# Performance work log

Hardware: AMD Instinct MI355X
Metric: run time of the kernel (lower is better)

The kernel has to match this reference:

```python
import jax, jax.numpy as jnp
import numpy as np

N, E, D, H, L, G, C = 50000, 800000, 128, 128, 3, 128, 10
BN_EPS = 1e-5


def setup_inputs() -> dict:
    key = jax.random.key(0)
    ks = jax.random.split(key, 16)
    inp = {
        "x": jax.random.normal(ks[0], (N, D), dtype=jnp.float32),
        "node_centrality": jax.random.uniform(ks[1], (N,), dtype=jnp.float32),
        "edge_centrality": jax.random.uniform(ks[2], (E,), dtype=jnp.float32),
        # stacked per-layer MLP params (in == hidden so stackable)
        "W1": jax.random.normal(ks[3], (L, D, H), dtype=jnp.float32) * 0.05,
        "b1": jnp.zeros((L, H), dtype=jnp.float32),
        "g1": jnp.ones((L, H), dtype=jnp.float32),
        "be1": jnp.zeros((L, H), dtype=jnp.float32),
        "W2": jax.random.normal(ks[4], (L, H, H), dtype=jnp.float32) * 0.05,
        "b2": jnp.zeros((L, H), dtype=jnp.float32),
        "Wc": jax.random.normal(ks[5], (H, C), dtype=jnp.float32) * 0.05,
        "bc": jnp.zeros((C,), dtype=jnp.float32),
        "edge_index": jax.random.randint(ks[6], (2, E), 0, N, dtype=jnp.int64),
        "batch": jnp.sort(jax.random.randint(ks[7], (N,), 0, G, dtype=jnp.int64)),
    }
    return inp


def _gin_forward(x, node_centrality, edge_centrality, W1, b1, g1, be1, W2, b2, Wc, bc, edge_index, batch):
    src, dst = edge_index[0], edge_index[1]  # x_j = x[src], aggregate at dst
    ec = edge_centrality[:, None]
    nc = node_centrality[:, None]
    for l in range(L):
        # message: gather + scale by edge centrality; aggr='add': scatter-add
        msg = x[src] * ec                                      # [E, H]
        agg = jax.ops.segment_sum(msg, dst, num_segments=N)    # [N, H]
        h = agg * nc + x                                       # (1 + eps) * x_r, eps = 0
        # MLP([in, hidden, hidden]): Linear -> BatchNorm(train) -> ReLU -> Linear
        h = h @ W1[l] + b1[l]
        mu = h.mean(axis=0)
        var = h.var(axis=0)  # biased, matches BN training stats
        h = (h - mu) * jax.lax.rsqrt(var + BN_EPS) * g1[l] + be1[l]
        h = jax.nn.relu(h)
        h = h @ W2[l] + b2[l]
        x = jax.nn.relu(h)  # outer .relu() in GIN.forward
    # global mean pool over graphs
    sums = jax.ops.segment_sum(x, batch, num_segments=G)           # [G, H]
    cnt = jax.ops.segment_sum(jnp.ones((N,), x.dtype), batch, num_segments=G)
    pooled = sums / jnp.maximum(cnt, 1.0)[:, None]
    return pooled @ Wc + bc  # [G, C]


def reference(x, edge_index, batch, node_centrality, edge_centrality, W1, b1, g1, be1, W2, b2, Wc, bc):
    return _gin_forward(x, node_centrality, edge_centrality, W1, b1, g1, be1, W2, b2, Wc, bc, edge_index, batch)
```

## Files before the change

### kernel.cpp

```cpp
#include <hip/hip_runtime.h>
#include <hip/hip_fp16.h>

#define Nn 50000
#define Ee 800000
#define HD 128
#define Ll 3
#define Gg 128
#define Cc 10
#define BN_EPS 1e-5f
#define NBLK1 782
#define NPART 1564
#define PPAD 1600
#define NSCB 49

typedef __attribute__((ext_vector_type(8))) __bf16 bf16x8;
typedef __attribute__((ext_vector_type(4))) __bf16 bf16x4;
typedef __attribute__((ext_vector_type(2))) __bf16 bf16x2;
typedef __attribute__((ext_vector_type(4))) float f32x4;

__global__ void k_deg(const int* __restrict__ dst, int* __restrict__ deg) {
  int i = blockIdx.x * blockDim.x + threadIdx.x;
  int base = i * 4;
  if (base >= Ee) return;
#pragma unroll
  for (int j = 0; j < 4; ++j) {
    int e = base + j;
    if (e < Ee) atomicAdd(&deg[dst[e]], 1);
  }
}

__global__ void k_scan1(const int* __restrict__ deg, int* __restrict__ offs,
                        int* __restrict__ bsum) {
  __shared__ int b0[1024], b1[1024];
  int tid = threadIdx.x;
  int i = blockIdx.x * 1024 + tid;
  int v = (i < Nn) ? deg[i] : 0;
  int* cur = b0; int* nxt = b1;
  cur[tid] = v;
  __syncthreads();
  for (int off = 1; off < 1024; off <<= 1) {
    int s = cur[tid] + ((tid >= off) ? cur[tid - off] : 0);
    nxt[tid] = s;
    __syncthreads();
    int* t = cur; cur = nxt; nxt = t;
  }
  if (i < Nn) offs[i] = cur[tid] - v;
  if (tid == 1023) bsum[blockIdx.x] = cur[1023];
}

__global__ void k_scan2(const int* __restrict__ bsum, int* __restrict__ carry) {
  int lane = threadIdx.x;
  int v = (lane < NSCB) ? bsum[lane] : 0;
  int s = v;
  for (int off = 1; off < 64; off <<= 1) {
    int t = __shfl_up(s, off, 64);
    if (lane >= off) s += t;
  }
  if (lane < NSCB) carry[lane] = s - v;
}

__global__ void k_scan3(const int* __restrict__ carry, int* __restrict__ offs,
                        int* __restrict__ cursor) {
  int i = blockIdx.x * 1024 + threadIdx.x;
  if (i < Nn) {
    int o = offs[i] + carry[blockIdx.x];
    offs[i] = o; cursor[i] = o;
  }
  if (i == 0) offs[Nn] = Ee;
}

__global__ void k_fill(const int* __restrict__ src, const int* __restrict__ dst,
                       const float* __restrict__ ec, int* __restrict__ cursor,
                       unsigned int* __restrict__ epk) {
  int i = blockIdx.x * blockDim.x + threadIdx.x;
  int base = i * 4;
  if (base >= Ee) return;
  int d[4], s[4], p[4]; unsigned short hb[4]; bool ok[4];
#pragma unroll
  for (int j = 0; j < 4; ++j) {
    int e = base + j;
    ok[j] = e < Ee;
    if (ok[j]) {
      d[j] = dst[e]; s[j] = src[e];
      hb[j] = __half_as_ushort(__float2half(ec[e]));
    }
  }
#pragma unroll
  for (int j = 0; j < 4; ++j)
    if (ok[j]) p[j] = atomicAdd(&cursor[d[j]], 1);
#pragma unroll
  for (int j = 0; j < 4; ++j)
    if (ok[j]) epk[p[j]] = ((unsigned int)s[j] << 16) | hb[j];
}

__global__ void k_xcast(const float* __restrict__ x, __bf16* __restrict__ xb) {
  int i = blockIdx.x * blockDim.x + threadIdx.x;
  int stride = gridDim.x * blockDim.x;
  const int n4 = Nn * 32;
  for (int t = i; t < n4; t += stride) {
    f32x4 v = ((const f32x4*)x)[t];
    bf16x4 b;
#pragma unroll
    for (int j = 0; j < 4; ++j) b[j] = (__bf16)v[j];
    ((bf16x4*)xb)[t] = b;
  }
}

__global__ void k_wprep(const float* __restrict__ W1, const float* __restrict__ W2,
                        __bf16* __restrict__ wtHi, __bf16* __restrict__ wtLo) {
  int mat = blockIdx.x >> 3;
  int chunk = blockIdx.x & 7;
  const float* W = (mat < 3) ? (W1 + mat * 16384) : (W2 + (mat - 3) * 16384);
  __bf16* hi = wtHi + mat * 16384;
  __bf16* lo = wtLo + mat * 16384;
  for (int t = threadIdx.x; t < 2048; t += blockDim.x) {
    int idx = chunk * 2048 + t;
    int n = idx >> 7, k = idx & 127;
    float v = W[k * 128 + n];
    __bf16 h = (__bf16)v;
    hi[idx] = h;
    lo[idx] = (__bf16)(v - (float)h);
  }
}

__launch_bounds__(256)
__global__ void k_gemm1(const __bf16* __restrict__ xb, const float* __restrict__ nc,
                        const int* __restrict__ offs, const unsigned int* __restrict__ epk,
                        const __bf16* __restrict__ wtHi, const __bf16* __restrict__ wtLo,
                        const float* __restrict__ bias, __bf16* __restrict__ h1b,
                        float* __restrict__ partial) {
  __shared__ unsigned int Als[64 * 64];
  int tid = threadIdx.x;
  int w = tid >> 6, l = tid & 63;
  int row0 = blockIdx.x * 64;
  const unsigned int* x2 = (const unsigned int*)xb;

  for (int it = 0; it < 16; ++it) {
    int n = row0 + w * 16 + it;
    float sx = 0.f, sy = 0.f;
    if (n < Nn) {
      int beg = offs[n], end = offs[n + 1];
      float ax[8], ay[8];
#pragma unroll
      for (int t = 0; t < 8; ++t) { ax[t] = 0.f; ay[t] = 0.f; }
      int j = beg;
      for (; j + 7 < end; j += 8) {
        unsigned int e[8], v[8];
#pragma unroll
        for (int t = 0; t < 8; ++t) e[t] = epk[j + t];
#pragma unroll
        for (int t = 0; t < 8; ++t) v[t] = x2[(e[t] >> 16) * 64 + l];
#pragma unroll
        for (int t = 0; t < 8; ++t) {
          __half_raw h; h.x = (unsigned short)(e[t] & 0xffffu);
          float wv = __half2float(h);
          ax[t] = fmaf(__uint_as_float(v[t] << 16), wv, ax[t]);
          ay[t] = fmaf(__uint_as_float(v[t] & 0xffff0000u), wv, ay[t]);
        }
      }
      for (; j < end; ++j) {
        unsigned int e = epk[j];
        unsigned int v = x2[(e >> 16) * 64 + l];
        __half_raw h; h.x = (unsigned short)(e & 0xffffu);
        float wv = __half2float(h);
        ax[0] = fmaf(__uint_as_float(v << 16), wv, ax[0]);
        ay[0] = fmaf(__uint_as_float(v & 0xffff0000u), wv, ay[0]);
      }
      float gx = (ax[0] + ax[1]) + (ax[2] + ax[3]) + ((ax[4] + ax[5]) + (ax[6] + ax[7]));
      float gy = (ay[0] + ay[1]) + (ay[2] + ay[3]) + ((ay[4] + ay[5]) + (ay[6] + ay[7]));
      float ncv = nc[n];
      unsigned int xv = x2[n * 64 + l];
      sx = fmaf(gx, ncv, __uint_as_float(xv << 16));
      sy = fmaf(gy, ncv, __uint_as_float(xv & 0xffff0000u));
    }
    bf16x2 tpk; tpk[0] = (__bf16)sx; tpk[1] = (__bf16)sy;
    unsigned int o = *(unsigned int*)&tpk;
    int sw = (((l >> 2) ^ it) << 2) | (l & 3);
    Als[(w * 16 + it) * 64 + sw] = o;
  }
  __syncthreads();

  int wr = w >> 1, wc = w & 1;
  int l15 = l & 15, lg = l >> 4;
  int colw = wc * 64;

  f32x4 acc[2][4];
#pragma unroll
  for (int m = 0; m < 2; ++m)
#pragma unroll
    for (int n = 0; n < 4; ++n) acc[m][n] = (f32x4){0.f, 0.f, 0.f, 0.f};

#pragma unroll
  for (int ks = 0; ks < 4; ++ks) {
    int k0 = ks * 32 + lg * 8;
    bf16x8 a[2];
#pragma unroll
    for (int m = 0; m < 2; ++m) {
      int lr = wr * 32 + m * 16 + l15;
      int slot = (((ks * 4 + lg) ^ l15) << 2);
      a[m] = *(const bf16x8*)&Als[lr * 64 + slot];
    }
    bf16x8 bHi[4], bLo[4];
#pragma unroll
    for (int n = 0; n < 4; ++n) {
      int c = colw + n * 16 + l15;
      bHi[n] = *(const bf16x8*)(wtHi + c * 128 + k0);
      bLo[n] = *(const bf16x8*)(wtLo + c * 128 + k0);
    }
#pragma unroll
    for (int m = 0; m < 2; ++m)
#pragma unroll
      for (int n = 0; n < 4; ++n) {
        acc[m][n] = __builtin_amdgcn_mfma_f32_16x16x32_bf16(a[m], bHi[n], acc[m][n], 0, 0, 0);
        acc[m][n] = __builtin_amdgcn_mfma_f32_16x16x32_bf16(a[m], bLo[n], acc[m][n], 0, 0, 0);
      }
  }

  int row0w = row0 + wr * 32;
  float s[4] = {0.f, 0.f, 0.f, 0.f}, q[4] = {0.f, 0.f, 0.f, 0.f};
#pragma unroll
  for (int n = 0; n < 4; ++n) {
    int c = colw + n * 16 + l15;
    float bv = bias[c];
#pragma unroll
    for (int m = 0; m < 2; ++m) {
      int rbase = row0w + m * 16 + lg * 4;
#pragma unroll
      for (int r = 0; r < 4; ++r) {
        int rr = rbase + r;
        if (rr < Nn) {
          float o = acc[m][n][r] + bv;
          h1b[rr * 128 + c] = (__bf16)o;
          s[n] += o; q[n] += o * o;
        }
      }
    }
  }
#pragma unroll
  for (int n = 0; n < 4; ++n) {
    s[n] += __shfl_xor(s[n], 16, 64); q[n] += __shfl_xor(q[n], 16, 64);
    s[n] += __shfl_xor(s[n], 32, 64); q[n] += __shfl_xor(q[n], 32, 64);
  }
  if (lg == 0) {
    int slot = blockIdx.x * 2 + wr;
#pragma unroll
    for (int n = 0; n < 4; ++n) {
      int f = colw + n * 16 + l15;
      partial[f * PPAD + slot] = s[n];
      partial[(128 + f) * PPAD + slot] = q[n];
    }
  }
}

__global__ void k_bnfin(const float* __restrict__ partial,
                        const float* __restrict__ g1, const float* __restrict__ be1,
                        float* __restrict__ scaleA, float* __restrict__ shiftA) {
  __shared__ float ss[256], qq[256];
  int f = blockIdx.x, t = threadIdx.x;
  float s = 0.f, q = 0.f;
  for (int b = t; b < NPART; b += 256) {
    s += partial[f * PPAD + b];
    q += partial[(128 + f) * PPAD + b];
  }
  ss[t] = s; qq[t] = q;
  __syncthreads();
  for (int off = 128; off > 0; off >>= 1) {
    if (t < off) { ss[t] += ss[t + off]; qq[t] += qq[t + off]; }
    __syncthreads();
  }
  if (t == 0) {
    const float inv = 1.0f / (float)Nn;
    float mu = ss[0] * inv;
    float var = fmaxf(qq[0] * inv - mu * mu, 0.f);
    float rs = rsqrtf(var + BN_EPS);
    float sc = rs * g1[f];
    scaleA[f] = sc;
    shiftA[f] = be1[f] - mu * sc;
  }
}

__launch_bounds__(256)
__global__ void k_gemm2(const __bf16* __restrict__ h1b, const float* __restrict__ scaleA,
                        const float* __restrict__ shiftA,
                        const __bf16* __restrict__ wtHi, const __bf16* __restrict__ wtLo,
                        const float* __restrict__ bias, __bf16* __restrict__ xbout) {
  int tid = threadIdx.x;
  int w = tid >> 6, l = tid & 63;
  int wr = w >> 1, wc = w & 1;
  int row0 = blockIdx.x * 64 + wr * 32;
  int l15 = l & 15, lg = l >> 4;
  int colw = wc * 64;
  int krow = lg * 8;

  f32x4 acc[2][4];
#pragma unroll
  for (int m = 0; m < 2; ++m)
#pragma unroll
    for (int n = 0; n < 4; ++n) acc[m][n] = (f32x4){0.f, 0.f, 0.f, 0.f};

  int rowA[2]; bool rv[2];
#pragma unroll
  for (int m = 0; m < 2; ++m) {
    rowA[m] = row0 + m * 16 + l15;
    rv[m] = rowA[m] < Nn;
  }

#pragma unroll
  for (int ks = 0; ks < 4; ++ks) {
    int k0 = ks * 32 + krow;
    f32x4 sc0 = *(const f32x4*)(scaleA + k0), sc1 = *(const f32x4*)(scaleA + k0 + 4);
    f32x4 sh0 = *(const f32x4*)(shiftA + k0), sh1 = *(const f32x4*)(shiftA + k0 + 4);
    bf16x8 a[2];
#pragma unroll
    for (int m = 0; m < 2; ++m) {
      if (rv[m]) {
        bf16x8 hv = *(const bf16x8*)(h1b + rowA[m] * 128 + k0);
#pragma unroll
        for (int jj = 0; jj < 4; ++jj) {
          a[m][jj]     = (__bf16)fmaxf(fmaf((float)hv[jj],     sc0[jj], sh0[jj]), 0.f);
          a[m][4 + jj] = (__bf16)fmaxf(fmaf((float)hv[4 + jj], sc1[jj], sh1[jj]), 0.f);
        }
      } else {
#pragma unroll
        for (int jj = 0; jj < 8; ++jj) a[m][jj] = (__bf16)0.f;
      }
    }
    bf16x8 bHi[4], bLo[4];
#pragma unroll
    for (int n = 0; n < 4; ++n) {
      int c = colw + n * 16 + l15;
      bHi[n] = *(const bf16x8*)(wtHi + c * 128 + k0);
      bLo[n] = *(const bf16x8*)(wtLo + c * 128 + k0);
    }
#pragma unroll
    for (int m = 0; m < 2; ++m)
#pragma unroll
      for (int n = 0; n < 4; ++n) {
        acc[m][n] = __builtin_amdgcn_mfma_f32_16x16x32_bf16(a[m], bHi[n], acc[m][n], 0, 0, 0);
        acc[m][n] = __builtin_amdgcn_mfma_f32_16x16x32_bf16(a[m], bLo[n], acc[m][n], 0, 0, 0);
      }
  }

#pragma unroll
  for (int n = 0; n < 4; ++n) {
    int c = colw + n * 16 + l15;
    float bv = bias[c];
#pragma unroll
    for (int m = 0; m < 2; ++m) {
      int rbase = row0 + m * 16 + lg * 4;
#pragma unroll
      for (int r = 0; r < 4; ++r) {
        int rr = rbase + r;
        if (rr < Nn) xbout[rr * 128 + c] = (__bf16)fmaxf(acc[m][n][r] + bv, 0.f);
      }
    }
  }
}

#define PCH 64
__global__ void k_pool(const __bf16* __restrict__ xb, const int* __restrict__ batch,
                       float* __restrict__ pooled, float* __restrict__ gcnt) {
  int wid = threadIdx.x >> 6, lane = threadIdx.x & 63;
  int w = blockIdx.x * 4 + wid;
  int n0 = w * PCH;
  if (n0 >= Nn) return;
  int n1 = (n0 + PCH < Nn) ? n0 + PCH : Nn;
  const unsigned int* x2 = (const unsigned int*)xb;
  float2 acc = make_float2(0.f, 0.f);
  int cur = batch[n0];
  int cnt = 0;
  for (int n = n0; n < n1; ++n) {
    int g = batch[n];
    if (g != cur) {
      atomicAdd(&pooled[cur * 128 + lane * 2 + 0], acc.x);
      atomicAdd(&pooled[cur * 128 + lane * 2 + 1], acc.y);
      if (lane == 0) atomicAdd(&gcnt[cur], (float)cnt);
      acc = make_float2(0.f, 0.f); cnt = 0; cur = g;
    }
    unsigned int v = x2[n * 64 + lane];
    acc.x += __uint_as_float(v << 16);
    acc.y += __uint_as_float(v & 0xffff0000u);
    ++cnt;
  }
  atomicAdd(&pooled[cur * 128 + lane * 2 + 0], acc.x);
  atomicAdd(&pooled[cur * 128 + lane * 2 + 1], acc.y);
  if (lane == 0) atomicAdd(&gcnt[cur], (float)cnt);
}

__global__ void k_head(const float* __restrict__ pooled, const float* __restrict__ gcnt,
                       const float* __restrict__ Wc, const float* __restrict__ bc,
                       float* __restrict__ out) {
  __shared__ float p[128];
  int g = blockIdx.x, tid = threadIdx.x;
  p[tid] = pooled[g * 128 + tid] / fmaxf(gcnt[g], 1.0f);
  __syncthreads();
  if (tid < Cc) {
    float acc = bc[tid];
    for (int k = 0; k < 128; ++k) acc = fmaf(p[k], Wc[k * Cc + tid], acc);
    out[g * Cc + tid] = acc;
  }
}

extern "C" void kernel_launch(void* const* d_in, const int* in_sizes, int n_in,
                              void* d_out, int out_size, void* d_ws, size_t ws_size,
                              hipStream_t stream) {
  const float* x    = (const float*)d_in[0];
  const float* ncn  = (const float*)d_in[1];
  const float* ecn  = (const float*)d_in[2];
  const float* W1   = (const float*)d_in[3];
  const float* b1   = (const float*)d_in[4];
  const float* g1   = (const float*)d_in[5];
  const float* be1  = (const float*)d_in[6];
  const float* W2   = (const float*)d_in[7];
  const float* b2   = (const float*)d_in[8];
  const float* Wc   = (const float*)d_in[9];
  const float* bc   = (const float*)d_in[10];
  const int*   ei   = (const int*)d_in[11];
  const int*   batch= (const int*)d_in[12];
  const int* src  = ei;
  const int* dstp = ei + Ee;

  float* fws = (float*)d_ws;
  float* partial  = fws;
  float* scaleA   = partial + 256 * PPAD;
  float* shiftA   = scaleA + 128;
  float* pooled   = shiftA + 128;
  float* gcnt     = pooled + Gg * 128;
  int*   deg      = (int*)(gcnt + 128);
  int*   offs     = deg + Nn;
  int*   cursor   = offs + Nn + 64;
  int*   bsum     = cursor + Nn;
  int*   carry    = bsum + 64;
  unsigned int* epk = (unsigned int*)(carry + 64);
  __bf16* wtHi    = (__bf16*)(epk + Ee);
  __bf16* wtLo    = wtHi + 6 * 16384;
  __bf16* xb      = wtLo + 6 * 16384;
  __bf16* h1b     = xb + Nn * 128;

  k_wprep<<<48, 256, 0, stream>>>(W1, W2, wtHi, wtLo);
  k_xcast<<<2048, 256, 0, stream>>>(x, xb);
  hipMemsetAsync(deg, 0, Nn * sizeof(int), stream);
  k_deg<<<(Ee / 4 + 255) / 256, 256, 0, stream>>>(dstp, deg);
  k_scan1<<<NSCB, 1024, 0, stream>>>(deg, offs, bsum);
  k_scan2<<<1, 64, 0, stream>>>(bsum, carry);
  k_scan3<<<NSCB, 1024, 0, stream>>>(carry, offs, cursor);
  k_fill<<<(Ee / 4 + 255) / 256, 256, 0, stream>>>(src, dstp, ecn, cursor, epk);

  for (int l = 0; l < Ll; ++l) {
    k_gemm1<<<NBLK1, 256, 0, stream>>>(xb, ncn, offs, epk,
                                       wtHi + l * 16384, wtLo + l * 16384,
                                       b1 + l * 128, h1b, partial);
    k_bnfin<<<128, 256, 0, stream>>>(partial, g1 + l * 128, be1 + l * 128,
                                     scaleA, shiftA);
    k_gemm2<<<NBLK1, 256, 0, stream>>>(h1b, scaleA, shiftA,
                                       wtHi + (3 + l) * 16384, wtLo + (3 + l) * 16384,
                                       b2 + l * 128, xb);
  }

  hipMemsetAsync(pooled, 0, (Gg * 128 + 128) * sizeof(float), stream);
  k_pool<<<(Nn + PCH * 4 - 1) / (PCH * 4), 256, 0, stream>>>(xb, batch, pooled, gcnt);
  k_head<<<Gg, 128, 0, stream>>>(pooled, gcnt, Wc, bc, (float*)d_out);
}
```

Before: 592.8 us.

## Split aggregation from GEMM1 and halve GEMM row tiles

Neighbour aggregation moves out of the first GEMM into its own kernel, with one wave per node, and writes a bf16 aggregate buffer. GEMM1 then reads that buffer directly instead of staging tiles in LDS. Both GEMMs drop to 32-row tiles, which doubles the block count, and gain an occupancy hint in launch_bounds. The aim is better load balance and latency hiding for the irregular gather, and the cost is an extra round trip of an N×128 bf16 array through global memory on each layer.

```diff
diff --git a/kernel.cpp b/kernel.cpp
--- a/kernel.cpp
+++ b/kernel.cpp
@@ -8,9 +8,9 @@
 #define Gg 128
 #define Cc 10
 #define BN_EPS 1e-5f
-#define NBLK1 782
-#define NPART 1564
-#define PPAD 1600
+#define NBLKG 1563
+#define NPART 3126
+#define PPAD 3200
 #define NSCB 49
 
 typedef __attribute__((ext_vector_type(8))) __bf16 bf16x8;
@@ -123,82 +123,78 @@
   }
 }
 
-__launch_bounds__(256)
-__global__ void k_gemm1(const __bf16* __restrict__ xb, const float* __restrict__ nc,
-                        const int* __restrict__ offs, const unsigned int* __restrict__ epk,
+__global__ void k_agg(const __bf16* __restrict__ xb, const float* __restrict__ nc,
+                      const int* __restrict__ offs, const unsigned int* __restrict__ epk,
+                      __bf16* __restrict__ aggb) {
+  int wid = threadIdx.x >> 6, lane = threadIdx.x & 63;
+  int n = blockIdx.x * 4 + wid;
+  if (n >= Nn) return;
+  int beg = offs[n], end = offs[n + 1];
+  const unsigned int* x2 = (const unsigned int*)xb;
+  float ax[8], ay[8];
+#pragma unroll
+  for (int t = 0; t < 8; ++t) { ax[t] = 0.f; ay[t] = 0.f; }
+  int j = beg;
+  for (; j + 7 < end; j += 8) {
+    unsigned int e[8], v[8];
+#pragma unroll
+    for (int t = 0; t < 8; ++t) e[t] = epk[j + t];
+#pragma unroll
+    for (int t = 0; t < 8; ++t) v[t] = x2[(e[t] >> 16) * 64 + lane];
+#pragma unroll
+    for (int t = 0; t < 8; ++t) {
+      __half_raw h; h.x = (unsigned short)(e[t] & 0xffffu);
+      float w = __half2float(h);
+      ax[t] = fmaf(__uint_as_float(v[t] << 16), w, ax[t]);
+      ay[t] = fmaf(__uint_as_float(v[t] & 0xffff0000u), w, ay[t]);
+    }
+  }
+  for (; j < end; ++j) {
+    unsigned int e = epk[j];
+    unsigned int v = x2[(e >> 16) * 64 + lane];
+    __half_raw h; h.x = (unsigned short)(e & 0xffffu);
+    float w = __half2float(h);
+    ax[0] = fmaf(__uint_as_float(v << 16), w, ax[0]);
+    ay[0] = fmaf(__uint_as_float(v & 0xffff0000u), w, ay[0]);
+  }
+  float gx = (ax[0] + ax[1]) + (ax[2] + ax[3]) + ((ax[4] + ax[5]) + (ax[6] + ax[7]));
+  float gy = (ay[0] + ay[1]) + (ay[2] + ay[3]) + ((ay[4] + ay[5]) + (ay[6] + ay[7]));
+  float ncv = nc[n];
+  unsigned int xv = x2[n * 64 + lane];
+  float sx = fmaf(gx, ncv, __uint_as_float(xv << 16));
+  float sy = fmaf(gy, ncv, __uint_as_float(xv & 0xffff0000u));
+  bf16x2 o; o[0] = (__bf16)sx; o[1] = (__bf16)sy;
+  ((bf16x2*)aggb)[n * 64 + lane] = o;
+}
+
+__launch_bounds__(256, 6)
+__global__ void k_gemm1(const __bf16* __restrict__ aggb,
                         const __bf16* __restrict__ wtHi, const __bf16* __restrict__ wtLo,
                         const float* __restrict__ bias, __bf16* __restrict__ h1b,
                         float* __restrict__ partial) {
-  __shared__ unsigned int Als[64 * 64];
   int tid = threadIdx.x;
   int w = tid >> 6, l = tid & 63;
-  int row0 = blockIdx.x * 64;
-  const unsigned int* x2 = (const unsigned int*)xb;
-
-  for (int it = 0; it < 16; ++it) {
-    int n = row0 + w * 16 + it;
-    float sx = 0.f, sy = 0.f;
-    if (n < Nn) {
-      int beg = offs[n], end = offs[n + 1];
-      float ax[8], ay[8];
-#pragma unroll
-      for (int t = 0; t < 8; ++t) { ax[t] = 0.f; ay[t] = 0.f; }
-      int j = beg;
-      for (; j + 7 < end; j += 8) {
-        unsigned int e[8], v[8];
-#pragma unroll
-        for (int t = 0; t < 8; ++t) e[t] = epk[j + t];
-#pragma unroll
-        for (int t = 0; t < 8; ++t) v[t] = x2[(e[t] >> 16) * 64 + l];
-#pragma unroll
-        for (int t = 0; t < 8; ++t) {
-          __half_raw h; h.x = (unsigned short)(e[t] & 0xffffu);
-          float wv = __half2float(h);
-          ax[t] = fmaf(__uint_as_float(v[t] << 16), wv, ax[t]);
-          ay[t] = fmaf(__uint_as_float(v[t] & 0xffff0000u), wv, ay[t]);
-        }
-      }
-      for (; j < end; ++j) {
-        unsigned int e = epk[j];
-        unsigned int v = x2[(e >> 16) * 64 + l];
-        __half_raw h; h.x = (unsigned short)(e & 0xffffu);
-        float wv = __half2float(h);
-        ax[0] = fmaf(__uint_as_float(v << 16), wv, ax[0]);
-        ay[0] = fmaf(__uint_as_float(v & 0xffff0000u), wv, ay[0]);
-      }
-      float gx = (ax[0] + ax[1]) + (ax[2] + ax[3]) + ((ax[4] + ax[5]) + (ax[6] + ax[7]));
-      float gy = (ay[0] + ay[1]) + (ay[2] + ay[3]) + ((ay[4] + ay[5]) + (ay[6] + ay[7]));
-      float ncv = nc[n];
-      unsigned int xv = x2[n * 64 + l];
-      sx = fmaf(gx, ncv, __uint_as_float(xv << 16));
-      sy = fmaf(gy, ncv, __uint_as_float(xv & 0xffff0000u));
-    }
-    bf16x2 tpk; tpk[0] = (__bf16)sx; tpk[1] = (__bf16)sy;
-    unsigned int o = *(unsigned int*)&tpk;
-    int sw = (((l >> 2) ^ it) << 2) | (l & 3);
-    Als[(w * 16 + it) * 64 + sw] = o;
-  }
-  __syncthreads();
-
   int wr = w >> 1, wc = w & 1;
+  int row0 = blockIdx.x * 32 + wr * 16;
   int l15 = l & 15, lg = l >> 4;
   int colw = wc * 64;
-
-  f32x4 acc[2][4];
-#pragma unroll
-  for (int m = 0; m < 2; ++m)
-#pragma unroll
-    for (int n = 0; n < 4; ++n) acc[m][n] = (f32x4){0.f, 0.f, 0.f, 0.f};
+  int krow = lg * 8;
+
+  f32x4 acc[4];
+#pragma unroll
+  for (int n = 0; n < 4; ++n) acc[n] = (f32x4){0.f, 0.f, 0.f, 0.f};
+
+  int rowA = row0 + l15;
+  bool rv = rowA < Nn;
 
 #pragma unroll
   for (int ks = 0; ks < 4; ++ks) {
-    int k0 = ks * 32 + lg * 8;
-    bf16x8 a[2];
-#pragma unroll
-    for (int m = 0; m < 2; ++m) {
-      int lr = wr * 32 + m * 16 + l15;
-      int slot = (((ks * 4 + lg) ^ l15) << 2);
-      a[m] = *(const bf16x8*)&Als[lr * 64 + slot];
+    int k0 = ks * 32 + krow;
+    bf16x8 a;
+    if (rv) a = *(const bf16x8*)(aggb + rowA * 128 + k0);
+    else {
+#pragma unroll
+      for (int jj = 0; jj < 8; ++jj) a[jj] = (__bf16)0.f;
     }
     bf16x8 bHi[4], bLo[4];
 #pragma unroll
@@ -208,31 +204,25 @@
       bLo[n] = *(const bf16x8*)(wtLo + c * 128 + k0);
     }
 #pragma unroll
-    for (int m = 0; m < 2; ++m)
-#pragma unroll
-      for (int n = 0; n < 4; ++n) {
-        acc[m][n] = __builtin_amdgcn_mfma_f32_16x16x32_bf16(a[m], bHi[n], acc[m][n], 0, 0, 0);
-        acc[m][n] = __builtin_amdgcn_mfma_f32_16x16x32_bf16(a[m], bLo[n], acc[m][n], 0, 0, 0);
-      }
-  }
-
-  int row0w = row0 + wr * 32;
+    for (int n = 0; n < 4; ++n) {
+      acc[n] = __builtin_amdgcn_mfma_f32_16x16x32_bf16(a, bHi[n], acc[n], 0, 0, 0);
+      acc[n] = __builtin_amdgcn_mfma_f32_16x16x32_bf16(a, bLo[n], acc[n], 0, 0, 0);
+    }
+  }
+
   float s[4] = {0.f, 0.f, 0.f, 0.f}, q[4] = {0.f, 0.f, 0.f, 0.f};
 #pragma unroll
   for (int n = 0; n < 4; ++n) {
     int c = colw + n * 16 + l15;
     float bv = bias[c];
-#pragma unroll
-    for (int m = 0; m < 2; ++m) {
-      int rbase = row0w + m * 16 + lg * 4;
-#pragma unroll
-      for (int r = 0; r < 4; ++r) {
-        int rr = rbase + r;
-        if (rr < Nn) {
-          float o = acc[m][n][r] + bv;
-          h1b[rr * 128 + c] = (__bf16)o;
-          s[n] += o; q[n] += o * o;
-        }
+    int rbase = row0 + lg * 4;
+#pragma unroll
+    for (int r = 0; r < 4; ++r) {
+      int rr = rbase + r;
+      if (rr < Nn) {
+        float o = acc[n][r] + bv;
+        h1b[rr * 128 + c] = (__bf16)o;
+        s[n] += o; q[n] += o * o;
       }
     }
   }
@@ -279,7 +269,7 @@
   }
 }
 
-__launch_bounds__(256)
+__launch_bounds__(256, 6)
 __global__ void k_gemm2(const __bf16* __restrict__ h1b, const float* __restrict__ scaleA,
                         const float* __restrict__ shiftA,
                         const __bf16* __restrict__ wtHi, const __bf16* __restrict__ wtLo,
@@ -287,43 +277,34 @@
   int tid = threadIdx.x;
   int w = tid >> 6, l = tid & 63;
   int wr = w >> 1, wc = w & 1;
-  int row0 = blockIdx.x * 64 + wr * 32;
+  int row0 = blockIdx.x * 32 + wr * 16;
   int l15 = l & 15, lg = l >> 4;
   int colw = wc * 64;
   int krow = lg * 8;
 
-  f32x4 acc[2][4];
-#pragma unroll
-  for (int m = 0; m < 2; ++m)
-#pragma unroll
-    for (int n = 0; n < 4; ++n) acc[m][n] = (f32x4){0.f, 0.f, 0.f, 0.f};
-
-  int rowA[2]; bool rv[2];
-#pragma unroll
-  for (int m = 0; m < 2; ++m) {
-    rowA[m] = row0 + m * 16 + l15;
-    rv[m] = rowA[m] < Nn;
-  }
+  f32x4 acc[4];
+#pragma unroll
+  for (int n = 0; n < 4; ++n) acc[n] = (f32x4){0.f, 0.f, 0.f, 0.f};
+
+  int rowA = row0 + l15;
+  bool rv = rowA < Nn;
 
 #pragma unroll
   for (int ks = 0; ks < 4; ++ks) {
     int k0 = ks * 32 + krow;
     f32x4 sc0 = *(const f32x4*)(scaleA + k0), sc1 = *(const f32x4*)(scaleA + k0 + 4);
     f32x4 sh0 = *(const f32x4*)(shiftA + k0), sh1 = *(const f32x4*)(shiftA + k0 + 4);
-    bf16x8 a[2];
-#pragma unroll
-    for (int m = 0; m < 2; ++m) {
-      if (rv[m]) {
-        bf16x8 hv = *(const bf16x8*)(h1b + rowA[m] * 128 + k0);
-#pragma unroll
-        for (int jj = 0; jj < 4; ++jj) {
-          a[m][jj]     = (__bf16)fmaxf(fmaf((float)hv[jj],     sc0[jj], sh0[jj]), 0.f);
-          a[m][4 + jj] = (__bf16)fmaxf(fmaf((float)hv[4 + jj], sc1[jj], sh1[jj]), 0.f);
-        }
-      } else {
-#pragma unroll
-        for (int jj = 0; jj < 8; ++jj) a[m][jj] = (__bf16)0.f;
+    bf16x8 a;
+    if (rv) {
+      bf16x8 hv = *(const bf16x8*)(h1b + rowA * 128 + k0);
+#pragma unroll
+      for (int jj = 0; jj < 4; ++jj) {
+        a[jj]     = (__bf16)fmaxf(fmaf((float)hv[jj],     sc0[jj], sh0[jj]), 0.f);
+        a[4 + jj] = (__bf16)fmaxf(fmaf((float)hv[4 + jj], sc1[jj], sh1[jj]), 0.f);
       }
+    } else {
+#pragma unroll
+      for (int jj = 0; jj < 8; ++jj) a[jj] = (__bf16)0.f;
     }
     bf16x8 bHi[4], bLo[4];
 #pragma unroll
@@ -333,26 +314,21 @@
       bLo[n] = *(const bf16x8*)(wtLo + c * 128 + k0);
     }
 #pragma unroll
-    for (int m = 0; m < 2; ++m)
-#pragma unroll
-      for (int n = 0; n < 4; ++n) {
-        acc[m][n] = __builtin_amdgcn_mfma_f32_16x16x32_bf16(a[m], bHi[n], acc[m][n], 0, 0, 0);
-        acc[m][n] = __builtin_amdgcn_mfma_f32_16x16x32_bf16(a[m], bLo[n], acc[m][n], 0, 0, 0);
-      }
+    for (int n = 0; n < 4; ++n) {
+      acc[n] = __builtin_amdgcn_mfma_f32_16x16x32_bf16(a, bHi[n], acc[n], 0, 0, 0);
+      acc[n] = __builtin_amdgcn_mfma_f32_16x16x32_bf16(a, bLo[n], acc[n], 0, 0, 0);
+    }
   }
 
 #pragma unroll
   for (int n = 0; n < 4; ++n) {
     int c = colw + n * 16 + l15;
     float bv = bias[c];
-#pragma unroll
-    for (int m = 0; m < 2; ++m) {
-      int rbase = row0 + m * 16 + lg * 4;
-#pragma unroll
-      for (int r = 0; r < 4; ++r) {
-        int rr = rbase + r;
-        if (rr < Nn) xbout[rr * 128 + c] = (__bf16)fmaxf(acc[m][n][r] + bv, 0.f);
-      }
+    int rbase = row0 + lg * 4;
+#pragma unroll
+    for (int r = 0; r < 4; ++r) {
+      int rr = rbase + r;
+      if (rr < Nn) xbout[rr * 128 + c] = (__bf16)fmaxf(acc[n][r] + bv, 0.f);
     }
   }
 }
@@ -435,7 +411,8 @@
   __bf16* wtHi    = (__bf16*)(epk + Ee);
   __bf16* wtLo    = wtHi + 6 * 16384;
   __bf16* xb      = wtLo + 6 * 16384;
-  __bf16* h1b     = xb + Nn * 128;
+  __bf16* aggb    = xb + Nn * 128;
+  __bf16* h1b     = aggb + Nn * 128;
 
   k_wprep<<<48, 256, 0, stream>>>(W1, W2, wtHi, wtLo);
   k_xcast<<<2048, 256, 0, stream>>>(x, xb);
@@ -447,12 +424,13 @@
   k_fill<<<(Ee / 4 + 255) / 256, 256, 0, stream>>>(src, dstp, ecn, cursor, epk);
 
   for (int l = 0; l < Ll; ++l) {
-    k_gemm1<<<NBLK1, 256, 0, stream>>>(xb, ncn, offs, epk,
+    k_agg<<<(Nn + 3) / 4, 256, 0, stream>>>(xb, ncn, offs, epk, aggb);
+    k_gemm1<<<NBLKG, 256, 0, stream>>>(aggb,
                                        wtHi + l * 16384, wtLo + l * 16384,
                                        b1 + l * 128, h1b, partial);
     k_bnfin<<<128, 256, 0, stream>>>(partial, g1 + l * 128, be1 + l * 128,
                                      scaleA, shiftA);
-    k_gemm2<<<NBLK1, 256, 0, stream>>>(h1b, scaleA, shiftA,
+    k_gemm2<<<NBLKG, 256, 0, stream>>>(h1b, scaleA, shiftA,
                                        wtHi + (3 + l) * 16384, wtLo + (3 + l) * 16384,
                                        b2 + l * 128, xb);
   }
```

After: 596.8 us. No clear change (+0.7%).
